# Performance work log

Hardware: AMD Instinct MI355X
Metric: run time of the kernel (lower is better)

Reference implementation:

```python
import jax, jax.numpy as jnp
import numpy as np

T, K, D = 8192, 1024, 1024
START, STOP = K - 2, K - 1
NEG = -10000.0


def setup_inputs() -> dict:
    key = jax.random.key(0)
    ks = jax.random.split(key, 7)
    feats = jax.random.normal(ks[0], (T, K), jnp.float32)          # emission scores per utterance
    reps = jax.random.normal(ks[1], (T, D), jnp.float32)           # utterance representations (out_dict)
    spk_change = jax.random.randint(ks[2], (T,), 0, 2).astype(jnp.int32)  # speaker-change flag per step
    w_spk_change = jax.random.normal(ks[3], (2 * D,), jnp.float32)
    w_spk_unchange = jax.random.normal(ks[4], (2 * D,), jnp.float32)
    ti = jax.random.normal(ks[5], (K, K), jnp.float32)
    ta = jax.random.normal(ks[6], (K, K), jnp.float32)
    # CRF constraint init: nothing transitions INTO START, nothing transitions FROM STOP
    ti = ti.at[START, :].set(NEG).at[:, STOP].set(NEG)
    ta = ta.at[START, :].set(NEG).at[:, STOP].set(NEG)
    return dict(feats=feats, reps=reps, w_spk_change=w_spk_change,
                w_spk_unchange=w_spk_unchange, transitions_inter=ti,
                transitions_intra=ta, spk_change=spk_change)


def reference(feats, reps, w_spk_change, w_spk_unchange,
              transitions_inter, transitions_intra, spk_change):
    T_, K_ = feats.shape
    # concat(repr[i-1], repr[i]); at i==0 the code duplicates repr[0]
    prev = jnp.concatenate([reps[:1], reps[:-1]], axis=0)          # [T, D]
    cat = jnp.concatenate([prev, reps], axis=1)                    # [T, 2D]
    a_change = jax.nn.sigmoid(cat @ w_spk_change)                  # [T]
    a_unchange = jax.nn.sigmoid(cat @ w_spk_unchange)              # [T]
    # i==0 or same speaker -> unchange gate; speaker change (i>0) -> change gate
    use_change = spk_change.astype(bool) & (jnp.arange(T_) > 0)
    gate = jnp.where(use_change, a_change, a_unchange)             # [T]

    init = jnp.full((K_,), NEG, jnp.float32).at[START].set(0.0)

    def step(fv, xs):
        feat, g = xs                                               # feat: [K], g: scalar
        trans = g * transitions_inter + (1.0 - g) * transitions_intra  # [K_next, K_prev]
        # next_tag_var[next, prev] = fv[prev] + trans[next, prev] + emit[next]
        fv_new = jax.nn.logsumexp(fv[None, :] + trans + feat[:, None], axis=1)
        return fv_new, None

    fv, _ = jax.lax.scan(step, init, (feats, gate))

    # terminal: unchange gate on duplicated last representation, STOP row
    cat_last = jnp.concatenate([reps[-1], reps[-1]])               # [2D]
    g_t = jax.nn.sigmoid(cat_last @ w_spk_unchange)
    terminal = fv + g_t * transitions_inter[STOP] + (1.0 - g_t) * transitions_intra[STOP]
    return jax.nn.logsumexp(terminal)                              # log partition (scalar)
```

## Files before the change

### kernel.cpp

```cpp
#include <hip/hip_runtime.h>
#include <stdint.h>

#define T_STEPS 8192
#define K_TAGS 1024
#define D_DIM 1024
#define START_TAG 1022
#define STOP_TAG 1023
#define NEGV (-10000.0f)
#define LOG2E 1.4426950408889634f
#define LN2 0.6931471805599453f

#define NBLK 128
#define ROWS_PB 8
#define PREV_PT 8

__device__ __forceinline__ unsigned long long ld_agent_u64(const unsigned long long* p) {
  return __hip_atomic_load(p, __ATOMIC_RELAXED, __HIP_MEMORY_SCOPE_AGENT);
}
__device__ __forceinline__ void st_agent_u64(unsigned long long* p, unsigned long long v) {
  __hip_atomic_store(p, v, __ATOMIC_RELAXED, __HIP_MEMORY_SCOPE_AGENT);
}

__global__ void init_ws_kernel(unsigned long long* fvbuf, int* bmax) {
  int i = blockIdx.x * blockDim.x + threadIdx.x;
  if (i < 2 * K_TAGS) fvbuf[i] = 0ull;
  if (i == 0) *bmax = 0;
}

__global__ __launch_bounds__(256) void gate_kernel(
    const float* __restrict__ reps, const float* __restrict__ wc,
    const float* __restrict__ wu, const int* __restrict__ spk,
    float* __restrict__ gate, float* __restrict__ g_term) {
  int t = blockIdx.x;
  int tid = threadIdx.x;
  const float* cur;
  const float* prv;
  if (t < T_STEPS) {
    cur = reps + (size_t)t * D_DIM;
    prv = reps + (size_t)(t > 0 ? t - 1 : 0) * D_DIM;
  } else {
    cur = reps + (size_t)(T_STEPS - 1) * D_DIM;
    prv = cur;
  }
  float sc = 0.f, su = 0.f;
  for (int d = tid; d < D_DIM; d += 256) {
    float rp = prv[d], rc = cur[d];
    sc += rp * wc[d] + rc * wc[D_DIM + d];
    su += rp * wu[d] + rc * wu[D_DIM + d];
  }
#pragma unroll
  for (int off = 32; off; off >>= 1) {
    sc += __shfl_down(sc, off);
    su += __shfl_down(su, off);
  }
  __shared__ float lc[4], lu[4];
  int wid = tid >> 6;
  if ((tid & 63) == 0) { lc[wid] = sc; lu[wid] = su; }
  __syncthreads();
  if (tid == 0) {
    float dc = lc[0] + lc[1] + lc[2] + lc[3];
    float du = lu[0] + lu[1] + lu[2] + lu[3];
    if (t < T_STEPS) {
      bool uc = (t > 0) && (spk[t] != 0);
      float x = uc ? dc : du;
      gate[t] = 1.0f / (1.0f + __expf(-x));
    } else {
      *g_term = 1.0f / (1.0f + __expf(-du));
    }
  }
}

__global__ __launch_bounds__(256) void bmax_kernel(
    const float* __restrict__ ti, const float* __restrict__ ta, int* bmax) {
  size_t i = (size_t)blockIdx.x * blockDim.x + threadIdx.x;
  size_t n = (size_t)K_TAGS * K_TAGS;
  float m = 0.f;
  for (size_t j = i; j < n; j += (size_t)gridDim.x * blockDim.x)
    m = fmaxf(m, fmaxf(ti[j], ta[j]));
#pragma unroll
  for (int off = 32; off; off >>= 1) m = fmaxf(m, __shfl_xor(m, off));
  if ((threadIdx.x & 63) == 0) atomicMax(bmax, __float_as_int(m));
}

__global__ __launch_bounds__(1024) void crf_kernel(
    const float* __restrict__ feats, const float* __restrict__ ti,
    const float* __restrict__ ta, const float* __restrict__ gate,
    const float* __restrict__ g_term_p, const int* __restrict__ bmax_p,
    unsigned long long* fvbuf, float* __restrict__ out) {
  const int b = blockIdx.x;
  const int tid = threadIdx.x;
  const int lane = tid & 63;
  const int wid = tid >> 6;
  const int rloc = tid >> 7;
  const int grow = b * ROWS_PB + rloc;
  const int pr0 = (tid & 127) * PREV_PT;

  __shared__ __align__(16) float fvs[K_TAGS];
  __shared__ float wredM[16];
  __shared__ float wredS[16];
  __shared__ float m2s;

  float ta2[PREV_PT], df2[PREV_PT];
  {
    const size_t mb = (size_t)grow * K_TAGS + pr0;
#pragma unroll
    for (int c = 0; c < PREV_PT; ++c) {
      float a = ta[mb + c];
      float i_ = ti[mb + c];
      ta2[c] = a * LOG2E;
      df2[c] = (i_ - a) * LOG2E;
    }
  }
  const float bmax2 = __int_as_float(*bmax_p) * LOG2E;

  if (tid < ROWS_PB) {
    int r = b * ROWS_PB + tid;
    float v = (r == START_TAG) ? 0.0f : NEGV * LOG2E;
    st_agent_u64(&fvbuf[r],
                 (1ull << 32) | (unsigned long long)__float_as_uint(v));
  }

  for (int t = 0; t < T_STEPS; ++t) {
    const int slot = t & 1;
    const unsigned want = (unsigned)(t + 1);
    const float g = gate[t];
    float featv = 0.f;
    if (tid < ROWS_PB)
      featv = feats[(size_t)t * K_TAGS + b * ROWS_PB + tid];

    unsigned long long* ep = &fvbuf[slot * K_TAGS + tid];
    unsigned long long u = ld_agent_u64(ep);
    while ((unsigned)(u >> 32) < want) {
      __builtin_amdgcn_s_sleep(1);
      u = ld_agent_u64(ep);
    }
    const float v = __uint_as_float((unsigned)u);

    float m = v;
#pragma unroll
    for (int off = 32; off; off >>= 1) m = fmaxf(m, __shfl_xor(m, off));
    if (lane == 0) wredM[wid] = m;
    __syncthreads();
    if (tid == 0) {
      float mm = wredM[0];
#pragma unroll
      for (int i = 1; i < 16; ++i) mm = fmaxf(mm, wredM[i]);
      m2s = mm + bmax2;
    }
    __syncthreads();
    const float M2 = m2s;
    fvs[tid] = v - M2;
    __syncthreads();

    const float4 f0 = *reinterpret_cast<const float4*>(&fvs[pr0]);
    const float4 f1 = *reinterpret_cast<const float4*>(&fvs[pr0 + 4]);
    const float fv8[8] = {f0.x, f0.y, f0.z, f0.w, f1.x, f1.y, f1.z, f1.w};
    float acc = 0.f;
#pragma unroll
    for (int c = 0; c < PREV_PT; ++c)
      acc += exp2f(__builtin_fmaf(g, df2[c], ta2[c]) + fv8[c]);
#pragma unroll
    for (int off = 32; off; off >>= 1) acc += __shfl_xor(acc, off);
    if (lane == 0) wredS[wid] = acc;
    __syncthreads();

    if (tid < ROWS_PB) {
      float s = wredS[tid * 2] + wredS[tid * 2 + 1];
      float fvnew = M2 + __log2f(s) + featv * LOG2E;
      st_agent_u64(&fvbuf[(slot ^ 1) * K_TAGS + b * ROWS_PB + tid],
                   ((unsigned long long)(unsigned)(t + 2) << 32) |
                       (unsigned long long)__float_as_uint(fvnew));
    }
  }

  if (b == 0) {
    const int slot = T_STEPS & 1;
    unsigned long long* ep = &fvbuf[slot * K_TAGS + tid];
    const unsigned want = (unsigned)(T_STEPS + 1);
    unsigned long long u = ld_agent_u64(ep);
    while ((unsigned)(u >> 32) < want) {
      __builtin_amdgcn_s_sleep(1);
      u = ld_agent_u64(ep);
    }
    const float v = __uint_as_float((unsigned)u);
    const float gt = *g_term_p;
    const float tis = ti[(size_t)STOP_TAG * K_TAGS + tid];
    const float tas = ta[(size_t)STOP_TAG * K_TAGS + tid];
    const float term2 = v + (tas + gt * (tis - tas)) * LOG2E;

    float m = term2;
#pragma unroll
    for (int off = 32; off; off >>= 1) m = fmaxf(m, __shfl_xor(m, off));
    if (lane == 0) wredM[wid] = m;
    __syncthreads();
    if (tid == 0) {
      float mm = wredM[0];
#pragma unroll
      for (int i = 1; i < 16; ++i) mm = fmaxf(mm, wredM[i]);
      m2s = mm;
    }
    __syncthreads();
    const float M2 = m2s;
    float e = exp2f(term2 - M2);
#pragma unroll
    for (int off = 32; off; off >>= 1) e += __shfl_xor(e, off);
    if (lane == 0) wredS[wid] = e;
    __syncthreads();
    if (tid == 0) {
      float s = 0.f;
#pragma unroll
      for (int i = 0; i < 16; ++i) s += wredS[i];
      out[0] = (M2 + __log2f(s)) * LN2;
    }
  }
}

extern "C" void kernel_launch(void* const* d_in, const int* in_sizes, int n_in,
                              void* d_out, int out_size, void* d_ws, size_t ws_size,
                              hipStream_t stream) {
  (void)in_sizes; (void)n_in; (void)out_size; (void)ws_size;
  const float* feats = (const float*)d_in[0];
  const float* reps  = (const float*)d_in[1];
  const float* wc    = (const float*)d_in[2];
  const float* wu    = (const float*)d_in[3];
  const float* ti    = (const float*)d_in[4];
  const float* ta    = (const float*)d_in[5];
  const int*   spk   = (const int*)d_in[6];
  float* out = (float*)d_out;

  unsigned long long* fvbuf = (unsigned long long*)d_ws;
  float* gate  = (float*)((char*)d_ws + 2 * K_TAGS * sizeof(unsigned long long));
  float* gterm = gate + T_STEPS;
  int*   bmax  = (int*)(gterm + 1);

  init_ws_kernel<<<dim3(8), dim3(256), 0, stream>>>(fvbuf, bmax);
  gate_kernel<<<dim3(T_STEPS + 1), dim3(256), 0, stream>>>(reps, wc, wu, spk, gate, gterm);
  bmax_kernel<<<dim3(512), dim3(256), 0, stream>>>(ti, ta, bmax);
  crf_kernel<<<dim3(NBLK), dim3(1024), 0, stream>>>(feats, ti, ta, gate, gterm, bmax, fvbuf, out);
}
```

Measured before the change: 17.88 ms.

## Restructure CRF recurrence to one wave per row with fewer block barriers

The CRF scan now runs 256 blocks of 256 threads, each wave owning one output row and reducing over all 1024 previous tags by itself. Per-step block synchronisation drops from four barriers to one, the exchanged fv values are double-buffered in shared memory, and the spin-wait polls without sleeping. The gate kernel is also rewritten so one wave with float4 loads handles each timestep. The aim is to shorten the serial per-step latency of the 8192-step recurrence. The cost is more spinning blocks polling global memory, plus the need for all 256 blocks to be co-resident.

```diff
diff --git a/kernel.cpp b/kernel.cpp
--- a/kernel.cpp
+++ b/kernel.cpp
@@ -10,9 +10,9 @@
 #define LOG2E 1.4426950408889634f
 #define LN2 0.6931471805599453f
 
-#define NBLK 128
-#define ROWS_PB 8
-#define PREV_PT 8
+#define NBLK 256
+#define ROWS_PB 4
+#define C8 8
 
 __device__ __forceinline__ unsigned long long ld_agent_u64(const unsigned long long* p) {
   return __hip_atomic_load(p, __ATOMIC_RELAXED, __HIP_MEMORY_SCOPE_AGENT);
@@ -31,41 +31,40 @@
     const float* __restrict__ reps, const float* __restrict__ wc,
     const float* __restrict__ wu, const int* __restrict__ spk,
     float* __restrict__ gate, float* __restrict__ g_term) {
-  int t = blockIdx.x;
-  int tid = threadIdx.x;
-  const float* cur;
-  const float* prv;
-  if (t < T_STEPS) {
-    cur = reps + (size_t)t * D_DIM;
-    prv = reps + (size_t)(t > 0 ? t - 1 : 0) * D_DIM;
-  } else {
-    cur = reps + (size_t)(T_STEPS - 1) * D_DIM;
-    prv = cur;
-  }
+  const int gw = (int)((blockIdx.x * blockDim.x + threadIdx.x) >> 6);
+  const int lane = threadIdx.x & 63;
+  if (gw > T_STEPS) return;
+  const int tcur = (gw < T_STEPS) ? gw : (T_STEPS - 1);
+  const int tprv = (gw < T_STEPS) ? (gw > 0 ? gw - 1 : 0) : (T_STEPS - 1);
+  const float* cur = reps + (size_t)tcur * D_DIM;
+  const float* prv = reps + (size_t)tprv * D_DIM;
   float sc = 0.f, su = 0.f;
-  for (int d = tid; d < D_DIM; d += 256) {
-    float rp = prv[d], rc = cur[d];
-    sc += rp * wc[d] + rc * wc[D_DIM + d];
-    su += rp * wu[d] + rc * wu[D_DIM + d];
+#pragma unroll
+  for (int c = 0; c < 4; ++c) {
+    const int d = lane * 4 + c * 256;
+    float4 rp = *(const float4*)(prv + d);
+    float4 rc = *(const float4*)(cur + d);
+    float4 w1 = *(const float4*)(wc + d);
+    float4 w2 = *(const float4*)(wc + D_DIM + d);
+    float4 w3 = *(const float4*)(wu + d);
+    float4 w4 = *(const float4*)(wu + D_DIM + d);
+    sc += rp.x * w1.x + rp.y * w1.y + rp.z * w1.z + rp.w * w1.w;
+    sc += rc.x * w2.x + rc.y * w2.y + rc.z * w2.z + rc.w * w2.w;
+    su += rp.x * w3.x + rp.y * w3.y + rp.z * w3.z + rp.w * w3.w;
+    su += rc.x * w4.x + rc.y * w4.y + rc.z * w4.z + rc.w * w4.w;
   }
 #pragma unroll
   for (int off = 32; off; off >>= 1) {
-    sc += __shfl_down(sc, off);
-    su += __shfl_down(su, off);
-  }
-  __shared__ float lc[4], lu[4];
-  int wid = tid >> 6;
-  if ((tid & 63) == 0) { lc[wid] = sc; lu[wid] = su; }
-  __syncthreads();
-  if (tid == 0) {
-    float dc = lc[0] + lc[1] + lc[2] + lc[3];
-    float du = lu[0] + lu[1] + lu[2] + lu[3];
-    if (t < T_STEPS) {
-      bool uc = (t > 0) && (spk[t] != 0);
-      float x = uc ? dc : du;
-      gate[t] = 1.0f / (1.0f + __expf(-x));
+    sc += __shfl_xor(sc, off);
+    su += __shfl_xor(su, off);
+  }
+  if (lane == 0) {
+    if (gw < T_STEPS) {
+      bool uc = (gw > 0) && (spk[gw] != 0);
+      float x = uc ? sc : su;
+      gate[gw] = 1.0f / (1.0f + __expf(-x));
     } else {
-      *g_term = 1.0f / (1.0f + __expf(-du));
+      *g_term = 1.0f / (1.0f + __expf(-su));
     }
   }
 }
@@ -82,7 +81,7 @@
   if ((threadIdx.x & 63) == 0) atomicMax(bmax, __float_as_int(m));
 }
 
-__global__ __launch_bounds__(1024) void crf_kernel(
+__global__ __launch_bounds__(256) void crf_kernel(
     const float* __restrict__ feats, const float* __restrict__ ti,
     const float* __restrict__ ta, const float* __restrict__ gate,
     const float* __restrict__ g_term_p, const int* __restrict__ bmax_p,
@@ -90,33 +89,34 @@
   const int b = blockIdx.x;
   const int tid = threadIdx.x;
   const int lane = tid & 63;
-  const int wid = tid >> 6;
-  const int rloc = tid >> 7;
-  const int grow = b * ROWS_PB + rloc;
-  const int pr0 = (tid & 127) * PREV_PT;
-
-  __shared__ __align__(16) float fvs[K_TAGS];
-  __shared__ float wredM[16];
-  __shared__ float wredS[16];
-  __shared__ float m2s;
-
-  float ta2[PREV_PT], df2[PREV_PT];
+  const int w = tid >> 6;
+  const int r = b * ROWS_PB + w;
+  const int e0 = tid * 4;
+
+  __shared__ __align__(16) float fvs[2][K_TAGS];
+  __shared__ float wredM[4];
+  __shared__ float wredS[4];
+
+  float ta2[16], df2[16];
   {
-    const size_t mb = (size_t)grow * K_TAGS + pr0;
-#pragma unroll
-    for (int c = 0; c < PREV_PT; ++c) {
-      float a = ta[mb + c];
-      float i_ = ti[mb + c];
-      ta2[c] = a * LOG2E;
-      df2[c] = (i_ - a) * LOG2E;
+    const float2* taP = reinterpret_cast<const float2*>(ta + (size_t)r * K_TAGS) + lane;
+    const float2* tiP = reinterpret_cast<const float2*>(ti + (size_t)r * K_TAGS) + lane;
+#pragma unroll
+    for (int c = 0; c < C8; ++c) {
+      float2 a = taP[64 * c];
+      float2 i_ = tiP[64 * c];
+      ta2[2 * c] = a.x * LOG2E;
+      df2[2 * c] = (i_.x - a.x) * LOG2E;
+      ta2[2 * c + 1] = a.y * LOG2E;
+      df2[2 * c + 1] = (i_.y - a.y) * LOG2E;
     }
   }
   const float bmax2 = __int_as_float(*bmax_p) * LOG2E;
 
   if (tid < ROWS_PB) {
-    int r = b * ROWS_PB + tid;
-    float v = (r == START_TAG) ? 0.0f : NEGV * LOG2E;
-    st_agent_u64(&fvbuf[r],
+    int rr = b * ROWS_PB + tid;
+    float v = (rr == START_TAG) ? 0.0f : NEGV * LOG2E;
+    st_agent_u64(&fvbuf[rr],
                  (1ull << 32) | (unsigned long long)__float_as_uint(v));
   }
 
@@ -125,91 +125,92 @@
     const unsigned want = (unsigned)(t + 1);
     const float g = gate[t];
     float featv = 0.f;
-    if (tid < ROWS_PB)
-      featv = feats[(size_t)t * K_TAGS + b * ROWS_PB + tid];
-
-    unsigned long long* ep = &fvbuf[slot * K_TAGS + tid];
-    unsigned long long u = ld_agent_u64(ep);
-    while ((unsigned)(u >> 32) < want) {
-      __builtin_amdgcn_s_sleep(1);
-      u = ld_agent_u64(ep);
-    }
-    const float v = __uint_as_float((unsigned)u);
-
-    float m = v;
+    if (lane == 0) featv = feats[(size_t)t * K_TAGS + r];
+
+    unsigned long long* ep = &fvbuf[slot * K_TAGS + e0];
+    unsigned long long u0 = ld_agent_u64(ep + 0);
+    unsigned long long u1 = ld_agent_u64(ep + 1);
+    unsigned long long u2 = ld_agent_u64(ep + 2);
+    unsigned long long u3 = ld_agent_u64(ep + 3);
+    while ((unsigned)(u0 >> 32) < want || (unsigned)(u1 >> 32) < want ||
+           (unsigned)(u2 >> 32) < want || (unsigned)(u3 >> 32) < want) {
+      u0 = ld_agent_u64(ep + 0);
+      u1 = ld_agent_u64(ep + 1);
+      u2 = ld_agent_u64(ep + 2);
+      u3 = ld_agent_u64(ep + 3);
+    }
+    const float v0 = __uint_as_float((unsigned)u0);
+    const float v1 = __uint_as_float((unsigned)u1);
+    const float v2 = __uint_as_float((unsigned)u2);
+    const float v3 = __uint_as_float((unsigned)u3);
+
+    *reinterpret_cast<float4*>(&fvs[slot][e0]) = make_float4(v0, v1, v2, v3);
+    float m = fmaxf(fmaxf(v0, v1), fmaxf(v2, v3));
 #pragma unroll
     for (int off = 32; off; off >>= 1) m = fmaxf(m, __shfl_xor(m, off));
-    if (lane == 0) wredM[wid] = m;
+    if (lane == 0) wredM[w] = m;
+    __syncthreads();
+    const float M2 =
+        fmaxf(fmaxf(wredM[0], wredM[1]), fmaxf(wredM[2], wredM[3])) + bmax2;
+
+    float acc = 0.f;
+    const float2* fp = reinterpret_cast<const float2*>(&fvs[slot][0]) + lane;
+#pragma unroll
+    for (int c = 0; c < C8; ++c) {
+      float2 f = fp[64 * c];
+      acc += exp2f(__builtin_fmaf(g, df2[2 * c], ta2[2 * c]) + (f.x - M2));
+      acc += exp2f(__builtin_fmaf(g, df2[2 * c + 1], ta2[2 * c + 1]) + (f.y - M2));
+    }
+#pragma unroll
+    for (int off = 32; off; off >>= 1) acc += __shfl_xor(acc, off);
+
+    if (lane == 0) {
+      float fvnew = M2 + __log2f(acc) + featv * LOG2E;
+      st_agent_u64(&fvbuf[(slot ^ 1) * K_TAGS + r],
+                   ((unsigned long long)(unsigned)(t + 2) << 32) |
+                       (unsigned long long)__float_as_uint(fvnew));
+    }
+  }
+
+  if (b == 0) {
+    const unsigned want = (unsigned)(T_STEPS + 1);
+    unsigned long long* ep = &fvbuf[(T_STEPS & 1) * K_TAGS + e0];
+    unsigned long long u0 = ld_agent_u64(ep + 0);
+    unsigned long long u1 = ld_agent_u64(ep + 1);
+    unsigned long long u2 = ld_agent_u64(ep + 2);
+    unsigned long long u3 = ld_agent_u64(ep + 3);
+    while ((unsigned)(u0 >> 32) < want || (unsigned)(u1 >> 32) < want ||
+           (unsigned)(u2 >> 32) < want || (unsigned)(u3 >> 32) < want) {
+      u0 = ld_agent_u64(ep + 0);
+      u1 = ld_agent_u64(ep + 1);
+      u2 = ld_agent_u64(ep + 2);
+      u3 = ld_agent_u64(ep + 3);
+    }
+    const float gt = *g_term_p;
+    float term[4];
+    const unsigned long long uu[4] = {u0, u1, u2, u3};
+#pragma unroll
+    for (int j = 0; j < 4; ++j) {
+      const int k = e0 + j;
+      float tis = ti[(size_t)STOP_TAG * K_TAGS + k];
+      float tas = ta[(size_t)STOP_TAG * K_TAGS + k];
+      term[j] = __uint_as_float((unsigned)uu[j]) +
+                (tas + gt * (tis - tas)) * LOG2E;
+    }
+    float m = fmaxf(fmaxf(term[0], term[1]), fmaxf(term[2], term[3]));
+#pragma unroll
+    for (int off = 32; off; off >>= 1) m = fmaxf(m, __shfl_xor(m, off));
+    if (lane == 0) wredM[w] = m;
+    __syncthreads();
+    const float M2 = fmaxf(fmaxf(wredM[0], wredM[1]), fmaxf(wredM[2], wredM[3]));
+    float e = exp2f(term[0] - M2) + exp2f(term[1] - M2) +
+              exp2f(term[2] - M2) + exp2f(term[3] - M2);
+#pragma unroll
+    for (int off = 32; off; off >>= 1) e += __shfl_xor(e, off);
+    if (lane == 0) wredS[w] = e;
     __syncthreads();
     if (tid == 0) {
-      float mm = wredM[0];
-#pragma unroll
-      for (int i = 1; i < 16; ++i) mm = fmaxf(mm, wredM[i]);
-      m2s = mm + bmax2;
-    }
-    __syncthreads();
-    const float M2 = m2s;
-    fvs[tid] = v - M2;
-    __syncthreads();
-
-    const float4 f0 = *reinterpret_cast<const float4*>(&fvs[pr0]);
-    const float4 f1 = *reinterpret_cast<const float4*>(&fvs[pr0 + 4]);
-    const float fv8[8] = {f0.x, f0.y, f0.z, f0.w, f1.x, f1.y, f1.z, f1.w};
-    float acc = 0.f;
-#pragma unroll
-    for (int c = 0; c < PREV_PT; ++c)
-      acc += exp2f(__builtin_fmaf(g, df2[c], ta2[c]) + fv8[c]);
-#pragma unroll
-    for (int off = 32; off; off >>= 1) acc += __shfl_xor(acc, off);
-    if (lane == 0) wredS[wid] = acc;
-    __syncthreads();
-
-    if (tid < ROWS_PB) {
-      float s = wredS[tid * 2] + wredS[tid * 2 + 1];
-      float fvnew = M2 + __log2f(s) + featv * LOG2E;
-      st_agent_u64(&fvbuf[(slot ^ 1) * K_TAGS + b * ROWS_PB + tid],
-                   ((unsigned long long)(unsigned)(t + 2) << 32) |
-                       (unsigned long long)__float_as_uint(fvnew));
-    }
-  }
-
-  if (b == 0) {
-    const int slot = T_STEPS & 1;
-    unsigned long long* ep = &fvbuf[slot * K_TAGS + tid];
-    const unsigned want = (unsigned)(T_STEPS + 1);
-    unsigned long long u = ld_agent_u64(ep);
-    while ((unsigned)(u >> 32) < want) {
-      __builtin_amdgcn_s_sleep(1);
-      u = ld_agent_u64(ep);
-    }
-    const float v = __uint_as_float((unsigned)u);
-    const float gt = *g_term_p;
-    const float tis = ti[(size_t)STOP_TAG * K_TAGS + tid];
-    const float tas = ta[(size_t)STOP_TAG * K_TAGS + tid];
-    const float term2 = v + (tas + gt * (tis - tas)) * LOG2E;
-
-    float m = term2;
-#pragma unroll
-    for (int off = 32; off; off >>= 1) m = fmaxf(m, __shfl_xor(m, off));
-    if (lane == 0) wredM[wid] = m;
-    __syncthreads();
-    if (tid == 0) {
-      float mm = wredM[0];
-#pragma unroll
-      for (int i = 1; i < 16; ++i) mm = fmaxf(mm, wredM[i]);
-      m2s = mm;
-    }
-    __syncthreads();
-    const float M2 = m2s;
-    float e = exp2f(term2 - M2);
-#pragma unroll
-    for (int off = 32; off; off >>= 1) e += __shfl_xor(e, off);
-    if (lane == 0) wredS[wid] = e;
-    __syncthreads();
-    if (tid == 0) {
-      float s = 0.f;
-#pragma unroll
-      for (int i = 0; i < 16; ++i) s += wredS[i];
+      float s = wredS[0] + wredS[1] + wredS[2] + wredS[3];
       out[0] = (M2 + __log2f(s)) * LN2;
     }
   }
@@ -234,7 +235,9 @@
   int*   bmax  = (int*)(gterm + 1);
 
   init_ws_kernel<<<dim3(8), dim3(256), 0, stream>>>(fvbuf, bmax);
-  gate_kernel<<<dim3(T_STEPS + 1), dim3(256), 0, stream>>>(reps, wc, wu, spk, gate, gterm);
+  gate_kernel<<<dim3((T_STEPS + 1 + 3) / 4), dim3(256), 0, stream>>>(
+      reps, wc, wu, spk, gate, gterm);
   bmax_kernel<<<dim3(512), dim3(256), 0, stream>>>(ti, ta, bmax);
-  crf_kernel<<<dim3(NBLK), dim3(1024), 0, stream>>>(feats, ti, ta, gate, gterm, bmax, fvbuf, out);
-}
+  crf_kernel<<<dim3(NBLK), dim3(256), 0, stream>>>(feats, ti, ta, gate, gterm,
+                                                   bmax, fvbuf, out);
+}
```

Measured after the change: 15.66 ms. -12.4%, faster.
